# Performance work log

Measured on AMD Instinct MI355X. Metric: run time of the kernel, lower is better.

## Reference

```python
import jax, jax.numpy as jnp
import numpy as np
import math


def setup_inputs() -> dict:
    key = jax.random.key(0)
    k_x, k_q, k_k, k_v, k_o = jax.random.split(key, 5)
    B, S, D_IN, H, D_K, D_V, D_OUT = 1, 4096, 512, 8, 64, 64, 512
    # torch.rand -> uniform[0,1); scaled by 0.02 to keep softmax unsaturated
    scale = 0.02
    return {
        "x": jax.random.normal(k_x, (B, S, D_IN), dtype=jnp.float32),
        "W_q": jax.random.uniform(k_q, (H, D_IN, D_K), dtype=jnp.float32) * scale,
        "W_k": jax.random.uniform(k_k, (H, D_IN, D_K), dtype=jnp.float32) * scale,
        "W_v": jax.random.uniform(k_v, (H, D_IN, D_V), dtype=jnp.float32) * scale,
        "W_o": jax.random.uniform(k_o, (H, D_V, D_OUT), dtype=jnp.float32) * scale,
    }


def reference(x, W_q, W_k, W_v, W_o):
    # x: [B,S,d_in]; W_q/W_k: [H,d_in,d_k]; W_v: [H,d_in,d_v]; W_o: [H,d_v,d_out]
    S = x.shape[-2]
    d_key = W_k.shape[-1]
    Q = jnp.einsum('hjk,blj->bhlk', W_q, x)   # [B,H,S,d_k]
    K = jnp.einsum('hjk,blj->bhlk', W_k, x)   # [B,H,S,d_k]
    V = jnp.einsum('hjk,blj->bhlk', W_v, x)   # [B,H,S,d_v]
    # causal mask: True where masked (strict upper triangle)
    mask = jnp.triu(jnp.ones((S, S), dtype=bool), k=1)  # [S,S]
    scores = jnp.einsum('bhik,bhjk->bhij', Q, K)        # [B,H,S,S]
    scores = jnp.where(mask, -jnp.inf, scores)
    # is_scaled=True: divide by sqrt(d_key) before softmax
    weights = jax.nn.softmax(scores / math.sqrt(d_key), axis=-1)
    weights = jnp.where(mask, 0.0, weights)
    values = jnp.einsum('bhij,bhjv->bhiv', weights, V)  # [B,H,S,d_v]
    return jnp.einsum('hvk,bhlv->blk', W_o, values)     # [B,S,d_out]
```

## Files before the change

### kernel.cpp

```cpp
#include <hip/hip_runtime.h>
#include <hip/hip_bf16.h>
#include <math.h>

#define S_LEN 4096
#define NH    8

typedef __attribute__((ext_vector_type(8))) short bf16x8;
typedef __attribute__((ext_vector_type(4))) short bf16x4;
typedef __attribute__((ext_vector_type(4))) float f32x4;
typedef __attribute__((ext_vector_type(16))) float f32x16;

#define QSCALE 0.18033688011112042f

#define WAIT_VM4 0x0F74
#define WAIT_VM0 0x0F70

__device__ __forceinline__ short f2bf(float f) {
    union { float f; unsigned u; } v; v.f = f;
    unsigned r = v.u + 0x7fffu + ((v.u >> 16) & 1u);
    return (short)(r >> 16);
}

__device__ __forceinline__ int pk2(float a, float b) {
    __hip_bfloat162 t = __float22bfloat162_rn(make_float2(a, b));
    union { __hip_bfloat162 h; int i; } u; u.h = t;
    return u.i;
}

__device__ __forceinline__ void gload16(const void* g, void* l) {
    __builtin_amdgcn_global_load_lds(
        (const __attribute__((address_space(1))) unsigned*)g,
        (__attribute__((address_space(3))) unsigned*)l, 16, 0, 0);
}

__device__ __forceinline__ void stage_tile(const short* gsrc, size_t gstride,
                                           short* tile, int t)
{
    const int wave = t >> 6, lane = t & 63;
    const int sub = lane >> 3;
    const int cg  = (lane & 7) ^ sub;
#pragma unroll
    for (int j = 0; j < 2; ++j) {
        const int chunk = wave * 2 + j;
        const int row = chunk * 8 + sub;
        gload16(gsrc + (size_t)row * gstride + cg * 8, tile + chunk * 512);
    }
}

__device__ __forceinline__ bf16x8 frag(const short* tile, int row, int cg) {
    return *(const bf16x8*)&tile[row * 64 + ((cg ^ (row & 7)) << 3)];
}

__device__ __forceinline__ void gemm_mainloop_512(
    const short* __restrict__ Arow, const short* __restrict__ Brow,
    short* As, short* Bs, f32x4 acc[4], int t)
{
    const int wave = t >> 6, lane = t & 63, n16 = lane & 15, quad = lane >> 4;
    stage_tile(Arow, 512, As, t);
    stage_tile(Brow, 512, Bs, t);
    for (int c = 0; c < 8; ++c) {
        const int cur = c & 1;
        __builtin_amdgcn_s_barrier();
        if (c < 7) {
            stage_tile(Arow + (c + 1) * 64, 512, As + (1 - cur) * 4096, t);
            stage_tile(Brow + (c + 1) * 64, 512, Bs + (1 - cur) * 4096, t);
            __builtin_amdgcn_s_waitcnt(WAIT_VM4);
        } else {
            __builtin_amdgcn_s_waitcnt(WAIT_VM0);
        }
        __builtin_amdgcn_s_barrier();
        const short* as = As + cur * 4096;
        const short* bs = Bs + cur * 4096;
#pragma unroll
        for (int kh = 0; kh < 2; ++kh) {
            const bf16x8 a = frag(as, wave * 16 + n16, kh * 4 + quad);
#pragma unroll
            for (int nt = 0; nt < 4; ++nt) {
                const bf16x8 b = frag(bs, nt * 16 + n16, kh * 4 + quad);
                acc[nt] = __builtin_amdgcn_mfma_f32_16x16x32_bf16(a, b, acc[nt], 0, 0, 0);
            }
        }
    }
}

__global__ __launch_bounds__(256) void prep_kernel(
    const float* __restrict__ x,
    const float* __restrict__ Wq, const float* __restrict__ Wk,
    const float* __restrict__ Wv, const float* __restrict__ Wo,
    short* __restrict__ xb, short* __restrict__ Wqkvt, short* __restrict__ Wot)
{
    __shared__ short T[64 * 66];
    const int b = blockIdx.x, t = threadIdx.x;
    if (b < 1024) {
        const size_t idx = (size_t)b * 2048 + t * 8;
        const float4 a = *(const float4*)&x[idx];
        const float4 c = *(const float4*)&x[idx + 4];
        bf16x8 o;
        o[0] = f2bf(a.x); o[1] = f2bf(a.y); o[2] = f2bf(a.z); o[3] = f2bf(a.w);
        o[4] = f2bf(c.x); o[5] = f2bf(c.y); o[6] = f2bf(c.z); o[7] = f2bf(c.w);
        *(bf16x8*)&xb[idx] = o;
        return;
    }
    const int c4 = (t & 15) * 4, rsub = t >> 4;
    const int orow = t >> 2, oc16 = (t & 3) * 16;
    if (b < 1216) {
        const int jj = b - 1024, g = jj >> 3, kb = jj & 7;
        const int which = g >> 3, h = g & 7;
        const float* W = ((which == 0) ? Wq : (which == 1) ? Wk : Wv) + (size_t)h * 512 * 64;
#pragma unroll
        for (int p = 0; p < 4; ++p) {
            const int row = p * 16 + rsub;
            const float4 v = *(const float4*)&W[(size_t)(kb * 64 + row) * 64 + c4];
            T[(c4 + 0) * 66 + row] = f2bf(v.x);
            T[(c4 + 1) * 66 + row] = f2bf(v.y);
            T[(c4 + 2) * 66 + row] = f2bf(v.z);
            T[(c4 + 3) * 66 + row] = f2bf(v.w);
        }
        __syncthreads();
        short* O = &Wqkvt[((size_t)g * 64 + orow) * 512 + kb * 64];
        *(bf16x8*)&O[oc16]     = *(const bf16x8*)&T[orow * 66 + oc16];
        *(bf16x8*)&O[oc16 + 8] = *(const bf16x8*)&T[orow * 66 + oc16 + 8];
    } else {
        const int jj = b - 1216, h = jj >> 3, nb = jj & 7;
        const float* W = Wo + (size_t)h * 64 * 512;
#pragma unroll
        for (int p = 0; p < 4; ++p) {
            const int row = p * 16 + rsub;
            const float4 v = *(const float4*)&W[(size_t)row * 512 + nb * 64 + c4];
            T[(c4 + 0) * 66 + row] = f2bf(v.x);
            T[(c4 + 1) * 66 + row] = f2bf(v.y);
            T[(c4 + 2) * 66 + row] = f2bf(v.z);
            T[(c4 + 3) * 66 + row] = f2bf(v.w);
        }
        __syncthreads();
        short* O = &Wot[((size_t)nb * 64 + orow) * 512 + h * 64];
        *(bf16x8*)&O[oc16]     = *(const bf16x8*)&T[orow * 66 + oc16];
        *(bf16x8*)&O[oc16 + 8] = *(const bf16x8*)&T[orow * 66 + oc16 + 8];
    }
}

__global__ __launch_bounds__(256) void qkv_gemm_kernel(
    const short* __restrict__ xb, const short* __restrict__ Wqkvt,
    short* __restrict__ Qg, short* __restrict__ Kg, short* __restrict__ Vtg)
{
    __shared__ short smem[16384];
    short* As = smem;
    short* Bs = smem + 8192;
    const int sblk = blockIdx.x, g = blockIdx.y;
    const int which = g >> 3, h = g & 7;
    const int t = threadIdx.x;
    const int wave = t >> 6, lane = t & 63, n16 = lane & 15, quad = lane >> 4;

    f32x4 acc[4] = {{0,0,0,0},{0,0,0,0},{0,0,0,0},{0,0,0,0}};
    gemm_mainloop_512(xb + (size_t)sblk * 64 * 512, Wqkvt + (size_t)g * 64 * 512,
                      As, Bs, acc, t);

    if (which < 2) {
        const float scale = (which == 0) ? QSCALE : 1.0f;
        short* O = ((which == 0) ? Qg : Kg) + (size_t)h * S_LEN * 64;
#pragma unroll
        for (int nt = 0; nt < 4; ++nt)
#pragma unroll
            for (int r = 0; r < 4; ++r) {
                const int s = sblk * 64 + wave * 16 + quad * 4 + r;
                O[(size_t)s * 64 + nt * 16 + n16] = f2bf(acc[nt][r] * scale);
            }
    } else {
        __syncthreads();
        short* Tr = smem;
#pragma unroll
        for (int nt = 0; nt < 4; ++nt)
#pragma unroll
            for (int r = 0; r < 4; ++r)
                Tr[(nt * 16 + n16) * 66 + wave * 16 + quad * 4 + r] = f2bf(acc[nt][r]);
        __syncthreads();
        short* O = Vtg + (size_t)h * 64 * S_LEN + sblk * 64;
        const int r4 = t >> 2, c16 = (t & 3) * 16;
        *(bf16x8*)&O[(size_t)r4 * S_LEN + c16]     = *(const bf16x8*)&Tr[r4 * 66 + c16];
        *(bf16x8*)&O[(size_t)r4 * S_LEN + c16 + 8] = *(const bf16x8*)&Tr[r4 * 66 + c16 + 8];
    }
}

__global__ __launch_bounds__(256) void out_gemm_kernel(
    const short* __restrict__ vals, const short* __restrict__ Wot, float* __restrict__ out)
{
    __shared__ short smem[16384];
    short* As = smem;
    short* Bs = smem + 8192;
    const int sblk = blockIdx.x, g = blockIdx.y;
    const int t = threadIdx.x;
    const int wave = t >> 6, lane = t & 63, n16 = lane & 15, quad = lane >> 4;

    f32x4 acc[4] = {{0,0,0,0},{0,0,0,0},{0,0,0,0},{0,0,0,0}};
    gemm_mainloop_512(vals + (size_t)sblk * 64 * 512, Wot + (size_t)g * 64 * 512,
                      As, Bs, acc, t);

#pragma unroll
    for (int nt = 0; nt < 4; ++nt)
#pragma unroll
        for (int r = 0; r < 4; ++r) {
            const int s = sblk * 64 + wave * 16 + quad * 4 + r;
            out[(size_t)s * 512 + g * 64 + nt * 16 + n16] = acc[nt][r];
        }
}

__global__ __launch_bounds__(256, 3) void attn_kernel(
    const short* __restrict__ Qg, const short* __restrict__ Kg,
    const short* __restrict__ Vtg, float* __restrict__ Opart, float* __restrict__ Lpart)
{
    __shared__ short Ks[2][4096];
    __shared__ short Vs[2][4096];
    __shared__ short Ps[4 * 32 * 72];

    const int id = blockIdx.x;
    const int h  = id & 7;
    const int c  = 79 - (id >> 3);
    int qs, j;
    if (c < 8)       { qs = c;                   j = 0; }
    else if (c < 24) { qs = 8 + ((c - 8) >> 1);  j = (c - 8) & 1; }
    else if (c < 48) { qs = 16 + (c - 24) / 3;   j = (c - 24) % 3; }
    else             { qs = 24 + ((c - 48) >> 2); j = (c - 48) & 3; }
    const int k0   = j * 16;
    const int kend = min(k0 + 16, 2 * qs + 2);

    const short* Kh  = Kg  + (size_t)h * S_LEN * 64;
    const short* Vth = Vtg + (size_t)h * 64 * S_LEN;

    const int t = threadIdx.x;
    const int wave = t >> 6, lane = t & 63, l31 = lane & 31, half = lane >> 5;
    const int qg = qs * 128 + wave * 32 + l31;

    const short* Qr = Qg + (size_t)h * S_LEN * 64 + (size_t)qg * 64;
    bf16x8 bq[4];
#pragma unroll
    for (int kc = 0; kc < 4; ++kc)
        bq[kc] = *(const bf16x8*)&Qr[kc * 16 + half * 8];

    bf16x8 ones;
#pragma unroll
    for (int i = 0; i < 8; ++i) ones[i] = (short)0x3F80;

    f32x16 z16;
#pragma unroll
    for (int r = 0; r < 16; ++r) z16[r] = 0.f;

    f32x16 oacc[2], lacc;
#pragma unroll
    for (int r = 0; r < 16; ++r) { oacc[0][r] = 0.f; oacc[1][r] = 0.f; lacc[r] = 0.f; }
    short* Pw = Ps + wave * (32 * 72);

    stage_tile(Kh + (size_t)k0 * 64 * 64, 64, Ks[0], t);
    stage_tile(Vth + k0 * 64, S_LEN, Vs[0], t);

    for (int kb = k0; kb < kend; ++kb) {
        const int cur = (kb - k0) & 1;
        __builtin_amdgcn_s_barrier();
        if (kb + 1 < kend) {
            stage_tile(Kh + (size_t)(kb + 1) * 64 * 64, 64, Ks[1 - cur], t);
            stage_tile(Vth + (kb + 1) * 64, S_LEN, Vs[1 - cur], t);
            __builtin_amdgcn_s_waitcnt(WAIT_VM4);
        } else {
            __builtin_amdgcn_s_waitcnt(WAIT_VM0);
        }
        __builtin_amdgcn_s_barrier();

        f32x16 sc0, sc1;
        {
            const bf16x8 a0 = frag(Ks[cur], l31,      half);
            const bf16x8 a1 = frag(Ks[cur], 32 + l31, half);
            sc0 = __builtin_amdgcn_mfma_f32_32x32x16_bf16(a0, bq[0], z16, 0, 0, 0);
            sc1 = __builtin_amdgcn_mfma_f32_32x32x16_bf16(a1, bq[0], z16, 0, 0, 0);
        }
#pragma unroll
        for (int kc = 1; kc < 4; ++kc) {
            const bf16x8 a0 = frag(Ks[cur], l31,      kc * 2 + half);
            const bf16x8 a1 = frag(Ks[cur], 32 + l31, kc * 2 + half);
            sc0 = __builtin_amdgcn_mfma_f32_32x32x16_bf16(a0, bq[kc], sc0, 0, 0, 0);
            sc1 = __builtin_amdgcn_mfma_f32_32x32x16_bf16(a1, bq[kc], sc1, 0, 0, 0);
        }

        if (kb * 64 + 63 > qg) {
#pragma unroll
            for (int r = 0; r < 16; ++r) {
                const int keyb = kb * 64 + (r & 3) + 8 * (r >> 2) + 4 * half;
                if (keyb > qg)      sc0[r] = -1e30f;
                if (keyb + 32 > qg) sc1[r] = -1e30f;
            }
        }

#pragma unroll
        for (int g2 = 0; g2 < 4; ++g2) {
            int2 w;
            w.x = pk2(__builtin_amdgcn_exp2f(sc0[4 * g2 + 0]),
                      __builtin_amdgcn_exp2f(sc0[4 * g2 + 1]));
            w.y = pk2(__builtin_amdgcn_exp2f(sc0[4 * g2 + 2]),
                      __builtin_amdgcn_exp2f(sc0[4 * g2 + 3]));
            *(int2*)&Pw[l31 * 72 + g2 * 8 + half * 4] = w;
            int2 w2;
            w2.x = pk2(__builtin_amdgcn_exp2f(sc1[4 * g2 + 0]),
                       __builtin_amdgcn_exp2f(sc1[4 * g2 + 1]));
            w2.y = pk2(__builtin_amdgcn_exp2f(sc1[4 * g2 + 2]),
                       __builtin_amdgcn_exp2f(sc1[4 * g2 + 3]));
            *(int2*)&Pw[l31 * 72 + 32 + g2 * 8 + half * 4] = w2;
        }
        __builtin_amdgcn_wave_barrier();

#pragma unroll
        for (int kc = 0; kc < 4; ++kc) {
            const bf16x8 bp = *(const bf16x8*)&Pw[l31 * 72 + kc * 16 + half * 8];
            const bf16x8 a0 = frag(Vs[cur], l31,      kc * 2 + half);
            const bf16x8 a1 = frag(Vs[cur], 32 + l31, kc * 2 + half);
            oacc[0] = __builtin_amdgcn_mfma_f32_32x32x16_bf16(a0, bp, oacc[0], 0, 0, 0);
            oacc[1] = __builtin_amdgcn_mfma_f32_32x32x16_bf16(a1, bp, oacc[1], 0, 0, 0);
            lacc    = __builtin_amdgcn_mfma_f32_32x32x16_bf16(ones, bp, lacc, 0, 0, 0);
        }
        __builtin_amdgcn_wave_barrier();
    }

    float* tileO = Opart + (size_t)(h * 80 + c) * (64 * 128);
    float* tileL = Lpart + (h * 80 + c) * 128;
    if (half == 0) tileL[wave * 32 + l31] = lacc[0];
#pragma unroll
    for (int mt = 0; mt < 2; ++mt)
#pragma unroll
        for (int r = 0; r < 16; ++r) {
            const int v = mt * 32 + (r & 3) + 8 * (r >> 2) + 4 * half;
            tileO[(v << 7) + wave * 32 + l31] = (mt ? oacc[1][r] : oacc[0][r]);
        }
}

__global__ __launch_bounds__(256) void combine_norm_kernel(
    const float* __restrict__ Opart, const float* __restrict__ Lpart,
    short* __restrict__ vals)
{
    __shared__ short T[128 * 66];
    const int id = blockIdx.x;
    const int h = id & 7, qs = id >> 3;
    int c0, nj;
    if (qs < 8)       { c0 = qs;                 nj = 1; }
    else if (qs < 16) { c0 = 8 + 2 * (qs - 8);   nj = 2; }
    else if (qs < 24) { c0 = 24 + 3 * (qs - 16); nj = 3; }
    else              { c0 = 48 + 4 * (qs - 24); nj = 4; }
    const int base = h * 80 + c0;

    const int t = threadIdx.x;
    const int q0 = (t & 31) * 4;
    const int vr = t >> 5;

    f32x4 L = {0, 0, 0, 0};
    for (int j = 0; j < nj; ++j)
        L += *(const f32x4*)&Lpart[(base + j) * 128 + q0];
    const f32x4 inv = {1.f / L[0], 1.f / L[1], 1.f / L[2], 1.f / L[3]};

#pragma unroll
    for (int pass = 0; pass < 8; ++pass) {
        const int v = vr + pass * 8;
        f32x4 s = {0, 0, 0, 0};
        for (int j = 0; j < nj; ++j)
            s += *(const f32x4*)&Opart[(size_t)(base + j) * 8192 + (v << 7) + q0];
        T[(q0 + 0) * 66 + v] = f2bf(s[0] * inv[0]);
        T[(q0 + 1) * 66 + v] = f2bf(s[1] * inv[1]);
        T[(q0 + 2) * 66 + v] = f2bf(s[2] * inv[2]);
        T[(q0 + 3) * 66 + v] = f2bf(s[3] * inv[3]);
    }
    __syncthreads();
    const int q = t >> 1, vh = (t & 1) * 32;
    const size_t row = (size_t)(qs * 128 + q) * 512 + h * 64 + vh;
#pragma unroll
    for (int u = 0; u < 4; ++u)
        *(bf16x8*)&vals[row + u * 8] = *(const bf16x8*)&T[q * 66 + vh + u * 8];
}

extern "C" void kernel_launch(void* const* d_in, const int* in_sizes, int n_in,
                              void* d_out, int out_size, void* d_ws, size_t ws_size,
                              hipStream_t stream)
{
    const float* x  = (const float*)d_in[0];
    const float* Wq = (const float*)d_in[1];
    const float* Wk = (const float*)d_in[2];
    const float* Wv = (const float*)d_in[3];
    const float* Wo = (const float*)d_in[4];
    float* out = (float*)d_out;

    short* xb    = (short*)d_ws;
    short* Wqkvt = xb + 2097152;
    short* Wot   = Wqkvt + 786432;
    short* Qg    = Wot + 262144;
    short* Kg    = Qg + 2097152;
    short* Vtg   = Kg + 2097152;
    short* vals  = Vtg + 2097152;
    float* Opart = (float*)(vals + 2097152);
    float* Lpart = Opart + (size_t)640 * 8192;

    prep_kernel<<<1280, 256, 0, stream>>>(x, Wq, Wk, Wv, Wo, xb, Wqkvt, Wot);
    qkv_gemm_kernel<<<dim3(64, 24), 256, 0, stream>>>(xb, Wqkvt, Qg, Kg, Vtg);
    attn_kernel<<<640, 256, 0, stream>>>(Qg, Kg, Vtg, Opart, Lpart);
    combine_norm_kernel<<<256, 256, 0, stream>>>(Opart, Lpart, vals);
    out_gemm_kernel<<<dim3(64, 8), 256, 0, stream>>>(vals, Wot, out);
}
```

Baseline: 135.2 us.

## Enlarge QKV and output GEMM tiles to 128x128 with 64x64 per-wave subtiles

Both projection GEMMs now compute 128x128 output tiles per block, each wave owning a 64x64 subtile with a 4x4 MFMA accumulator grid, in place of 64x64 tiles with 16x64 per wave. This raises operand reuse from LDS and global memory and cuts the block count by four. The cost is double the shared memory (64KB), more accumulator registers, and far fewer blocks (384 and 128), which may underfill the GPU's compute units. The V transpose epilogue now uses per-wave LDS regions with a wave barrier instead of a block-wide transpose.

```diff
diff --git a/kernel.cpp b/kernel.cpp
--- a/kernel.cpp
+++ b/kernel.cpp
@@ -12,6 +12,7 @@
 
 #define QSCALE 0.18033688011112042f
 
+#define WAIT_VM8 0x0F78
 #define WAIT_VM4 0x0F74
 #define WAIT_VM0 0x0F70
 
@@ -51,34 +52,46 @@
     return *(const bf16x8*)&tile[row * 64 + ((cg ^ (row & 7)) << 3)];
 }
 
-__device__ __forceinline__ void gemm_mainloop_512(
+__device__ __forceinline__ void gemm128_mainloop(
     const short* __restrict__ Arow, const short* __restrict__ Brow,
-    short* As, short* Bs, f32x4 acc[4], int t)
-{
-    const int wave = t >> 6, lane = t & 63, n16 = lane & 15, quad = lane >> 4;
-    stage_tile(Arow, 512, As, t);
-    stage_tile(Brow, 512, Bs, t);
+    short* smem, f32x4 acc[4][4], int t)
+{
+    const int w = t >> 6, lane = t & 63, n16 = lane & 15, quad = lane >> 4;
+    short* As = smem;
+    short* Bs = smem + 16384;
+    stage_tile(Arow,            512, As,        t);
+    stage_tile(Arow + 64 * 512, 512, As + 4096, t);
+    stage_tile(Brow,            512, Bs,        t);
+    stage_tile(Brow + 64 * 512, 512, Bs + 4096, t);
     for (int c = 0; c < 8; ++c) {
         const int cur = c & 1;
         __builtin_amdgcn_s_barrier();
         if (c < 7) {
-            stage_tile(Arow + (c + 1) * 64, 512, As + (1 - cur) * 4096, t);
-            stage_tile(Brow + (c + 1) * 64, 512, Bs + (1 - cur) * 4096, t);
-            __builtin_amdgcn_s_waitcnt(WAIT_VM4);
+            const int k = (c + 1) * 64;
+            stage_tile(Arow + k,            512, As + (1 - cur) * 8192,        t);
+            stage_tile(Arow + 64 * 512 + k, 512, As + (1 - cur) * 8192 + 4096, t);
+            stage_tile(Brow + k,            512, Bs + (1 - cur) * 8192,        t);
+            stage_tile(Brow + 64 * 512 + k, 512, Bs + (1 - cur) * 8192 + 4096, t);
+            __builtin_amdgcn_s_waitcnt(WAIT_VM8);
         } else {
             __builtin_amdgcn_s_waitcnt(WAIT_VM0);
         }
         __builtin_amdgcn_s_barrier();
-        const short* as = As + cur * 4096;
-        const short* bs = Bs + cur * 4096;
+        const short* as = As + cur * 8192 + (w & 1) * 4096;
+        const short* bs = Bs + cur * 8192 + (w >> 1) * 4096;
 #pragma unroll
         for (int kh = 0; kh < 2; ++kh) {
-            const bf16x8 a = frag(as, wave * 16 + n16, kh * 4 + quad);
-#pragma unroll
-            for (int nt = 0; nt < 4; ++nt) {
-                const bf16x8 b = frag(bs, nt * 16 + n16, kh * 4 + quad);
-                acc[nt] = __builtin_amdgcn_mfma_f32_16x16x32_bf16(a, b, acc[nt], 0, 0, 0);
-            }
+            bf16x8 a[4], b[4];
+#pragma unroll
+            for (int i = 0; i < 4; ++i) a[i] = frag(as, i * 16 + n16, kh * 4 + quad);
+#pragma unroll
+            for (int i = 0; i < 4; ++i) b[i] = frag(bs, i * 16 + n16, kh * 4 + quad);
+#pragma unroll
+            for (int rt = 0; rt < 4; ++rt)
+#pragma unroll
+                for (int nt = 0; nt < 4; ++nt)
+                    acc[rt][nt] = __builtin_amdgcn_mfma_f32_16x16x32_bf16(
+                        a[rt], b[nt], acc[rt][nt], 0, 0, 0);
         }
     }
 }
@@ -139,68 +152,90 @@
     }
 }
 
-__global__ __launch_bounds__(256) void qkv_gemm_kernel(
+__global__ __launch_bounds__(256, 2) void qkv_gemm_kernel(
     const short* __restrict__ xb, const short* __restrict__ Wqkvt,
     short* __restrict__ Qg, short* __restrict__ Kg, short* __restrict__ Vtg)
 {
-    __shared__ short smem[16384];
-    short* As = smem;
-    short* Bs = smem + 8192;
-    const int sblk = blockIdx.x, g = blockIdx.y;
-    const int which = g >> 3, h = g & 7;
+    __shared__ short smem[32768];
+    const int sblk = blockIdx.x, gp = blockIdx.y;
     const int t = threadIdx.x;
-    const int wave = t >> 6, lane = t & 63, n16 = lane & 15, quad = lane >> 4;
-
-    f32x4 acc[4] = {{0,0,0,0},{0,0,0,0},{0,0,0,0},{0,0,0,0}};
-    gemm_mainloop_512(xb + (size_t)sblk * 64 * 512, Wqkvt + (size_t)g * 64 * 512,
-                      As, Bs, acc, t);
+    const int w = t >> 6, lane = t & 63, n16 = lane & 15, quad = lane >> 4;
+
+    f32x4 acc[4][4];
+#pragma unroll
+    for (int i = 0; i < 4; ++i)
+#pragma unroll
+        for (int j = 0; j < 4; ++j) acc[i][j] = f32x4{0, 0, 0, 0};
+
+    gemm128_mainloop(xb + (size_t)sblk * 128 * 512,
+                     Wqkvt + (size_t)gp * 2 * 64 * 512, smem, acc, t);
+
+    const int g = 2 * gp + (w >> 1);
+    const int rbase = (w & 1) * 64;
+    const int which = gp >> 2;
 
     if (which < 2) {
         const float scale = (which == 0) ? QSCALE : 1.0f;
-        short* O = ((which == 0) ? Qg : Kg) + (size_t)h * S_LEN * 64;
-#pragma unroll
-        for (int nt = 0; nt < 4; ++nt)
+        short* O = ((which == 0) ? Qg : Kg) + (size_t)(g & 7) * S_LEN * 64;
+#pragma unroll
+        for (int rt = 0; rt < 4; ++rt)
 #pragma unroll
             for (int r = 0; r < 4; ++r) {
-                const int s = sblk * 64 + wave * 16 + quad * 4 + r;
-                O[(size_t)s * 64 + nt * 16 + n16] = f2bf(acc[nt][r] * scale);
+                const int s = sblk * 128 + rbase + rt * 16 + quad * 4 + r;
+#pragma unroll
+                for (int nt = 0; nt < 4; ++nt)
+                    O[(size_t)s * 64 + nt * 16 + n16] = f2bf(acc[rt][nt][r] * scale);
             }
     } else {
         __syncthreads();
-        short* Tr = smem;
-#pragma unroll
-        for (int nt = 0; nt < 4; ++nt)
-#pragma unroll
-            for (int r = 0; r < 4; ++r)
-                Tr[(nt * 16 + n16) * 66 + wave * 16 + quad * 4 + r] = f2bf(acc[nt][r]);
-        __syncthreads();
-        short* O = Vtg + (size_t)h * 64 * S_LEN + sblk * 64;
-        const int r4 = t >> 2, c16 = (t & 3) * 16;
-        *(bf16x8*)&O[(size_t)r4 * S_LEN + c16]     = *(const bf16x8*)&Tr[r4 * 66 + c16];
-        *(bf16x8*)&O[(size_t)r4 * S_LEN + c16 + 8] = *(const bf16x8*)&Tr[r4 * 66 + c16 + 8];
-    }
-}
-
-__global__ __launch_bounds__(256) void out_gemm_kernel(
+        short* Tr = smem + w * 4224;
+#pragma unroll
+        for (int rt = 0; rt < 4; ++rt)
+#pragma unroll
+            for (int nt = 0; nt < 4; ++nt)
+#pragma unroll
+                for (int r = 0; r < 4; ++r)
+                    Tr[(nt * 16 + n16) * 66 + rt * 16 + quad * 4 + r] = f2bf(acc[rt][nt][r]);
+        __builtin_amdgcn_wave_barrier();
+        const int h = g - 16;
+        short* O = Vtg + (size_t)h * 64 * S_LEN + sblk * 128 + rbase;
+        const int c16 = (lane & 3) * 16;
+#pragma unroll
+        for (int pass = 0; pass < 4; ++pass) {
+            const int row = pass * 16 + (lane >> 2);
+            *(bf16x8*)&O[(size_t)row * S_LEN + c16]     = *(const bf16x8*)&Tr[row * 66 + c16];
+            *(bf16x8*)&O[(size_t)row * S_LEN + c16 + 8] = *(const bf16x8*)&Tr[row * 66 + c16 + 8];
+        }
+    }
+}
+
+__global__ __launch_bounds__(256, 2) void out_gemm_kernel(
     const short* __restrict__ vals, const short* __restrict__ Wot, float* __restrict__ out)
 {
-    __shared__ short smem[16384];
-    short* As = smem;
-    short* Bs = smem + 8192;
-    const int sblk = blockIdx.x, g = blockIdx.y;
+    __shared__ short smem[32768];
+    const int sblk = blockIdx.x, gp = blockIdx.y;
     const int t = threadIdx.x;
-    const int wave = t >> 6, lane = t & 63, n16 = lane & 15, quad = lane >> 4;
-
-    f32x4 acc[4] = {{0,0,0,0},{0,0,0,0},{0,0,0,0},{0,0,0,0}};
-    gemm_mainloop_512(vals + (size_t)sblk * 64 * 512, Wot + (size_t)g * 64 * 512,
-                      As, Bs, acc, t);
-
-#pragma unroll
-    for (int nt = 0; nt < 4; ++nt)
+    const int w = t >> 6, lane = t & 63, n16 = lane & 15, quad = lane >> 4;
+
+    f32x4 acc[4][4];
+#pragma unroll
+    for (int i = 0; i < 4; ++i)
+#pragma unroll
+        for (int j = 0; j < 4; ++j) acc[i][j] = f32x4{0, 0, 0, 0};
+
+    gemm128_mainloop(vals + (size_t)sblk * 128 * 512,
+                     Wot + (size_t)gp * 128 * 512, smem, acc, t);
+
+    const int rbase = (w & 1) * 64;
+    const int cbase = gp * 128 + (w >> 1) * 64;
+#pragma unroll
+    for (int rt = 0; rt < 4; ++rt)
 #pragma unroll
         for (int r = 0; r < 4; ++r) {
-            const int s = sblk * 64 + wave * 16 + quad * 4 + r;
-            out[(size_t)s * 512 + g * 64 + nt * 16 + n16] = acc[nt][r];
+            const int s = sblk * 128 + rbase + rt * 16 + quad * 4 + r;
+#pragma unroll
+            for (int nt = 0; nt < 4; ++nt)
+                out[(size_t)s * 512 + cbase + nt * 16 + n16] = acc[rt][nt][r];
         }
 }
 
@@ -393,8 +428,8 @@
     float* Lpart = Opart + (size_t)640 * 8192;
 
     prep_kernel<<<1280, 256, 0, stream>>>(x, Wq, Wk, Wv, Wo, xb, Wqkvt, Wot);
-    qkv_gemm_kernel<<<dim3(64, 24), 256, 0, stream>>>(xb, Wqkvt, Qg, Kg, Vtg);
+    qkv_gemm_kernel<<<dim3(32, 12), 256, 0, stream>>>(xb, Wqkvt, Qg, Kg, Vtg);
     attn_kernel<<<640, 256, 0, stream>>>(Qg, Kg, Vtg, Opart, Lpart);
     combine_norm_kernel<<<256, 256, 0, stream>>>(Opart, Lpart, vals);
-    out_gemm_kernel<<<dim3(64, 8), 256, 0, stream>>>(vals, Wot, out);
-}
+    out_gemm_kernel<<<dim3(32, 4), 256, 0, stream>>>(vals, Wot, out);
+}
```

Result: no change. 137.6 us (+1.8%).

## Keep softmax probabilities in registers via lane shuffles instead of LDS round-trip

Applied to the files above, without the earlier changes.

Builds the PV MFMA B-operand directly from score registers by exchanging packed bf16 pairs across the two half-waves with shuffles, removing the per-wave P staging buffer in LDS and its wave barriers. The row sum is now accumulated with scalar adds in fp32 instead of an extra MFMA against a ones vector. The smaller register and LDS footprint lets the launch bound ask for 4 blocks per CU instead of 3. The trade-off is extra shuffle and select instructions, a different rounding of the denominator (fp32 of unrounded p rather than a sum of bf16 values), and possible register pressure or spills at the tighter occupancy target.

```diff
diff --git a/kernel.cpp b/kernel.cpp
--- a/kernel.cpp
+++ b/kernel.cpp
@@ -204,13 +204,12 @@
         }
 }
 
-__global__ __launch_bounds__(256, 3) void attn_kernel(
+__global__ __launch_bounds__(256, 4) void attn_kernel(
     const short* __restrict__ Qg, const short* __restrict__ Kg,
     const short* __restrict__ Vtg, float* __restrict__ Opart, float* __restrict__ Lpart)
 {
     __shared__ short Ks[2][4096];
     __shared__ short Vs[2][4096];
-    __shared__ short Ps[4 * 32 * 72];
 
     const int id = blockIdx.x;
     const int h  = id & 7;
@@ -236,18 +235,14 @@
     for (int kc = 0; kc < 4; ++kc)
         bq[kc] = *(const bf16x8*)&Qr[kc * 16 + half * 8];
 
-    bf16x8 ones;
-#pragma unroll
-    for (int i = 0; i < 8; ++i) ones[i] = (short)0x3F80;
-
     f32x16 z16;
 #pragma unroll
     for (int r = 0; r < 16; ++r) z16[r] = 0.f;
 
-    f32x16 oacc[2], lacc;
-#pragma unroll
-    for (int r = 0; r < 16; ++r) { oacc[0][r] = 0.f; oacc[1][r] = 0.f; lacc[r] = 0.f; }
-    short* Pw = Ps + wave * (32 * 72);
+    f32x16 oacc[2];
+#pragma unroll
+    for (int r = 0; r < 16; ++r) { oacc[0][r] = 0.f; oacc[1][r] = 0.f; }
+    float lsum = 0.f;
 
     stage_tile(Kh + (size_t)k0 * 64 * 64, 64, Ks[0], t);
     stage_tile(Vth + k0 * 64, S_LEN, Vs[0], t);
@@ -289,37 +284,42 @@
         }
 
 #pragma unroll
-        for (int g2 = 0; g2 < 4; ++g2) {
-            int2 w;
-            w.x = pk2(__builtin_amdgcn_exp2f(sc0[4 * g2 + 0]),
-                      __builtin_amdgcn_exp2f(sc0[4 * g2 + 1]));
-            w.y = pk2(__builtin_amdgcn_exp2f(sc0[4 * g2 + 2]),
-                      __builtin_amdgcn_exp2f(sc0[4 * g2 + 3]));
-            *(int2*)&Pw[l31 * 72 + g2 * 8 + half * 4] = w;
-            int2 w2;
-            w2.x = pk2(__builtin_amdgcn_exp2f(sc1[4 * g2 + 0]),
-                       __builtin_amdgcn_exp2f(sc1[4 * g2 + 1]));
-            w2.y = pk2(__builtin_amdgcn_exp2f(sc1[4 * g2 + 2]),
-                       __builtin_amdgcn_exp2f(sc1[4 * g2 + 3]));
-            *(int2*)&Pw[l31 * 72 + 32 + g2 * 8 + half * 4] = w2;
-        }
-        __builtin_amdgcn_wave_barrier();
-
-#pragma unroll
-        for (int kc = 0; kc < 4; ++kc) {
-            const bf16x8 bp = *(const bf16x8*)&Pw[l31 * 72 + kc * 16 + half * 8];
-            const bf16x8 a0 = frag(Vs[cur], l31,      kc * 2 + half);
-            const bf16x8 a1 = frag(Vs[cur], 32 + l31, kc * 2 + half);
-            oacc[0] = __builtin_amdgcn_mfma_f32_32x32x16_bf16(a0, bp, oacc[0], 0, 0, 0);
-            oacc[1] = __builtin_amdgcn_mfma_f32_32x32x16_bf16(a1, bp, oacc[1], 0, 0, 0);
-            lacc    = __builtin_amdgcn_mfma_f32_32x32x16_bf16(ones, bp, lacc, 0, 0, 0);
-        }
-        __builtin_amdgcn_wave_barrier();
-    }
+        for (int mt = 0; mt < 2; ++mt) {
+            float p[16];
+#pragma unroll
+            for (int r = 0; r < 16; ++r) {
+                p[r] = __builtin_amdgcn_exp2f(mt ? sc1[r] : sc0[r]);
+                lsum += p[r];
+            }
+#pragma unroll
+            for (int sub = 0; sub < 2; ++sub) {
+                const int d0lo = pk2(p[8 * sub + 0], p[8 * sub + 1]);
+                const int d0hi = pk2(p[8 * sub + 2], p[8 * sub + 3]);
+                const int d1lo = pk2(p[8 * sub + 4], p[8 * sub + 5]);
+                const int d1hi = pk2(p[8 * sub + 6], p[8 * sub + 7]);
+                const int send0 = half ? d0lo : d1lo;
+                const int send1 = half ? d0hi : d1hi;
+                const int rv0 = __shfl_xor(send0, 32);
+                const int rv1 = __shfl_xor(send1, 32);
+                union { int i[4]; bf16x8 v; } bp;
+                bp.i[0] = half ? rv0 : d0lo;
+                bp.i[1] = half ? rv1 : d0hi;
+                bp.i[2] = half ? d1lo : rv0;
+                bp.i[3] = half ? d1hi : rv1;
+                const int kc = 2 * mt + sub;
+                const bf16x8 a0 = frag(Vs[cur], l31,      kc * 2 + half);
+                const bf16x8 a1 = frag(Vs[cur], 32 + l31, kc * 2 + half);
+                oacc[0] = __builtin_amdgcn_mfma_f32_32x32x16_bf16(a0, bp.v, oacc[0], 0, 0, 0);
+                oacc[1] = __builtin_amdgcn_mfma_f32_32x32x16_bf16(a1, bp.v, oacc[1], 0, 0, 0);
+            }
+        }
+    }
+
+    lsum += __shfl_xor(lsum, 32);
 
     float* tileO = Opart + (size_t)(h * 80 + c) * (64 * 128);
     float* tileL = Lpart + (h * 80 + c) * 128;
-    if (half == 0) tileL[wave * 32 + l31] = lacc[0];
+    if (half == 0) tileL[wave * 32 + l31] = lsum;
 #pragma unroll
     for (int mt = 0; mt < 2; ++mt)
 #pragma unroll
```

Result: slower. 138.6 us (+2.6%).
